# Optimization experiments

Measured on AMD Instinct MI355X. Metric: run time of the kernel, lower is better.

Reference implementation:

```python
import jax, jax.numpy as jnp
import numpy as np
from jax.scipy.special import i0

IM_SIZE = (256, 256)
GRID_SIZE = (512, 512)
NUMPOINTS = 6
OS = GRID_SIZE[0] / IM_SIZE[0]
# Beatty et al. optimal Kaiser-Bessel shape parameter
BETA = float(np.pi * np.sqrt((NUMPOINTS / OS) ** 2 * (OS - 0.5) ** 2 - 0.8))


def _apod_1d(N, G):
    # 1/FT(kb kernel) scaling coefficients (de-apodization), static numpy
    x = np.arange(N) - N / 2.0
    arg = np.pi * NUMPOINTS * x / G
    t = BETA ** 2 - arg ** 2  # > 0 for this config
    ph = np.sinh(np.sqrt(t)) / np.sqrt(t)
    return (1.0 / ph).astype(np.float32)


def _kb(u):
    # Kaiser-Bessel interpolation kernel, support |u| <= NUMPOINTS/2
    x = 2.0 * u / NUMPOINTS
    t = 1.0 - x * x
    inside = t > 0
    t = jnp.where(inside, t, 0.0)
    return jnp.where(inside, i0(BETA * jnp.sqrt(t)), 0.0)


def setup_inputs():
    key = jax.random.key(0)
    k1, k2, k3 = jax.random.split(key, 3)
    B, M = 8, 131072
    image = jax.random.normal(k1, (B,) + IM_SIZE, dtype=jnp.float32)
    ktraj = (jax.random.uniform(k2, (B, 2, M), dtype=jnp.float32) * 2.0 - 1.0) * jnp.pi
    dcf = jax.random.uniform(k3, (B, M), dtype=jnp.float32)
    return {"image": image, "ktraj": ktraj, "dcf": dcf}


def _nufft(image, ktraj, dcf):
    B = image.shape[0]
    N1, N2 = IM_SIZE
    G1, G2 = GRID_SIZE
    J = NUMPOINTS
    # 1) de-apodization (scaling coefficients), separable per-dim
    a1 = jnp.asarray(_apod_1d(N1, G1))
    a2 = jnp.asarray(_apod_1d(N2, G2))
    img = image.astype(jnp.complex64) * (a1[:, None] * a2[None, :])
    # 2) centered zero-pad to oversampled grid, FFT with DC at bin 0
    p1, p2 = (G1 - N1) // 2, (G2 - N2) // 2
    grid = jnp.zeros((B, G1, G2), dtype=jnp.complex64).at[:, p1:p1 + N1, p2:p2 + N2].set(img)
    kgrid = jnp.fft.fft2(jnp.fft.ifftshift(grid, axes=(1, 2)))
    # 3) KB interpolation (gather) at non-uniform points
    tm1 = ktraj[:, 0] * (G1 / (2.0 * jnp.pi))  # (B,M) in grid units
    tm2 = ktraj[:, 1] * (G2 / (2.0 * jnp.pi))
    offs = jnp.arange(J, dtype=jnp.float32) - (J // 2 - 1)  # [-2..3]
    g1 = jnp.floor(tm1)[..., None] + offs  # (B,M,J) neighbor coords
    g2 = jnp.floor(tm2)[..., None] + offs
    w1 = _kb(tm1[..., None] - g1)
    w2 = _kb(tm2[..., None] - g2)
    i1 = jnp.mod(g1.astype(jnp.int32), G1)
    i2 = jnp.mod(g2.astype(jnp.int32), G2)
    lin = (i1[..., :, None] * G2 + i2[..., None, :]).reshape(B, -1)  # (B, M*J*J)
    vals = jnp.take_along_axis(kgrid.reshape(B, -1), lin, axis=1).reshape(B, -1, J, J)
    w = (w1[..., :, None] * w2[..., None, :]).astype(jnp.complex64)
    kdata = jnp.sum(vals * w, axis=(-1, -2))  # (B,M) complex
    kdata = kdata * dcf
    return jnp.stack([kdata.real, kdata.imag], axis=0)  # (2,B,M) float32


def reference(image, ktraj, dcf):
    return _nufft(image, ktraj, dcf)
```

## Files before the change

kernel.cpp:

```cpp
#include <hip/hip_runtime.h>
#include <math.h>

#define GSZ 512
#define NSZ 256
#define NBATCH 8
#define MPTS 131072
#define PI_F 3.14159265358979f
#define BETA_F 13.8551004f
#define BETA2_F (BETA_F * BETA_F)
#define RSQ2 0.70710678f
#define PADIDX(i) ((i) + ((i) >> 3))


__device__ __forceinline__ float apod(int i) {
    float x = (float)(i - 128);
    float arg = PI_F * 6.0f * x * (1.0f / 512.0f);
    float t = BETA2_F - arg * arg;
    float st = sqrtf(t);
    return st / sinhf(st);
}

__device__ __forceinline__ float kbw(float u) {
    float t = 1.0f - u * u * (1.0f / 9.0f);
    float x = BETA_F * sqrtf(fmaxf(t, 0.0f));
    float xc = fmaxf(x, 0.35f);
    float r = __builtin_amdgcn_rcpf(xc);
    float poly = 1.0f + r * (0.125f + r * 0.0703125f);
    float w = __expf(xc) * __builtin_amdgcn_rsqf(6.2831853f * xc) * poly;
    return (t > 0.0f) ? w : 0.0f;
}

template<int CTRL>
__device__ __forceinline__ float qdpp(float v) {
    int r = __builtin_amdgcn_mov_dpp(__float_as_int(v), CTRL, 0xF, 0xF, true);
    return __int_as_float(r);
}

struct __align__(8) F4 { float x, y, z, w; };

__device__ __forceinline__ float2 cadd(float2 a, float2 b){ return make_float2(a.x+b.x, a.y+b.y); }
__device__ __forceinline__ float2 csub(float2 a, float2 b){ return make_float2(a.x-b.x, a.y-b.y); }
__device__ __forceinline__ float2 cmul(float2 a, float2 b){ return make_float2(a.x*b.x-a.y*b.y, a.x*b.y+a.y*b.x); }
__device__ __forceinline__ float2 mul_negi(float2 a){ return make_float2(a.y, -a.x); }
__device__ __forceinline__ float2 mul_posi(float2 a){ return make_float2(-a.y, a.x); }
__device__ __forceinline__ float2 mul_w81(float2 a){ return make_float2(RSQ2*(a.x+a.y), RSQ2*(a.y-a.x)); }
__device__ __forceinline__ float2 mul_w83(float2 a){ return make_float2(RSQ2*(a.y-a.x), -RSQ2*(a.x+a.y)); }

__device__ __forceinline__ void dft8_combine(float2 E0, float2 E1, float2 E2, float2 E3,
                                             float2 O0, float2 O1, float2 O2, float2 O3,
                                             float2* y) {
    float2 c1 = mul_w81(O1), c2 = mul_negi(O2), c3 = mul_w83(O3);
    y[0] = cadd(E0, O0); y[4] = csub(E0, O0);
    y[1] = cadd(E1, c1); y[5] = csub(E1, c1);
    y[2] = cadd(E2, c2); y[6] = csub(E2, c2);
    y[3] = cadd(E3, c3); y[7] = csub(E3, c3);
}

__device__ __forceinline__ void dft8(const float2* x, float2* y) {
    float2 a0=x[0], a1=x[2], a2=x[4], a3=x[6];
    float2 b0=x[1], b1=x[3], b2=x[5], b3=x[7];
    float2 ta0=cadd(a0,a2), ta1=csub(a0,a2), ta2=cadd(a1,a3), ta3=csub(a1,a3);
    float2 E0=cadd(ta0,ta2), E2=csub(ta0,ta2);
    float2 E1=cadd(ta1, mul_negi(ta3)), E3=cadd(ta1, mul_posi(ta3));
    float2 tb0=cadd(b0,b2), tb1=csub(b0,b2), tb2=cadd(b1,b3), tb3=csub(b1,b3);
    float2 O0=cadd(tb0,tb2), O2=csub(tb0,tb2);
    float2 O1=cadd(tb1, mul_negi(tb3)), O3=cadd(tb1, mul_posi(tb3));
    dft8_combine(E0,E1,E2,E3,O0,O1,O2,O3,y);
}

__device__ __forceinline__ void dft8_pruned(float2 x0, float2 x1, float2 x6, float2 x7, float2* y) {
    float2 E0 = cadd(x0, x6), E2 = csub(x0, x6);
    float2 E1 = cadd(x0, mul_posi(x6)), E3 = cadd(x0, mul_negi(x6));
    float2 O0 = cadd(x1, x7), O2 = csub(x1, x7);
    float2 O1 = cadd(x1, mul_posi(x7)), O3 = cadd(x1, mul_negi(x7));
    dft8_combine(E0,E1,E2,E3,O0,O1,O2,O3,y);
}

template<int S>
__device__ __forceinline__ void twiddle8(int t, float2* y) {
    if (S < 2) {
        int j = (S == 0) ? t : (t >> 3);
        const float scale = (S == 0) ? (-2.0f*PI_F/512.0f) : (-2.0f*PI_F/64.0f);
        float theta = scale * (float)j;
        float sn, cs;
        __sincosf(theta, &sn, &cs);
        float2 w = make_float2(cs, sn), wq = w;
        y[1] = cmul(y[1], wq);
        #pragma unroll
        for (int q = 2; q < 8; ++q) { wq = cmul(wq, w); y[q] = cmul(y[q], wq); }
    }
}

__global__ __launch_bounds__(256) void pass1_rowfft(const float* __restrict__ image,
                                                    float2* __restrict__ T) {
    __shared__ float2 sm[2][4][578];
    int tid = threadIdx.x;
    int r = tid >> 6, t = tid & 63;
    int blk = blockIdx.x;
    int b = blk & 7;
    int g = blk >> 3;
    int rp = (g << 2) + r;
    int y = (rp < 128) ? rp : (rp + 256);
    int iy = (y < 128) ? (y + 128) : (y - 384);
    float ay = apod(iy);
    const float* irow = image + ((size_t)(b * NSZ + iy)) * NSZ;

    float2 y8[8];
    {
        int ix0 = t + 128, ix1 = t + 192, ix6 = t, ix7 = t + 64;
        float2 x0 = make_float2(irow[ix0] * ay * apod(ix0), 0.f);
        float2 x1 = make_float2(irow[ix1] * ay * apod(ix1), 0.f);
        float2 x6 = make_float2(irow[ix6] * ay * apod(ix6), 0.f);
        float2 x7 = make_float2(irow[ix7] * ay * apod(ix7), 0.f);
        dft8_pruned(x0, x1, x6, x7, y8);
        twiddle8<0>(t, y8);
    }
    float2* A  = sm[0][r];
    float2* Bf = sm[1][r];
    #pragma unroll
    for (int q = 0; q < 8; ++q) A[PADIDX((t << 3) + q)] = y8[q];
    __syncthreads();
    {
        float2 x[8];
        #pragma unroll
        for (int p = 0; p < 8; ++p) x[p] = A[PADIDX(t + (p << 6))];
        dft8(x, y8);
        twiddle8<1>(t, y8);
        int j = t >> 3, k = t & 7, base = k + (j << 6);
        #pragma unroll
        for (int q = 0; q < 8; ++q) Bf[PADIDX(base + (q << 3))] = y8[q];
    }
    __syncthreads();
    {
        float2 x[8];
        #pragma unroll
        for (int p = 0; p < 8; ++p) x[p] = Bf[PADIDX(t + (p << 6))];
        dft8(x, y8);
        float2* Trow = T + (((size_t)(b << 8) + rp) << 9);
        #pragma unroll
        for (int q = 0; q < 8; ++q) Trow[t + (q << 6)] = y8[q];
    }
}

__global__ __launch_bounds__(256) void pass2_colfft(const float2* __restrict__ T,
                                                    float2* __restrict__ kgrid) {
    __shared__ float2 B[8][578];
    int tid = threadIdx.x;
    int blk = blockIdx.x;
    int b = blk & 7;
    int colbase = (blk >> 3) << 3;
    const float2* Tb = T + ((size_t)b << 17);
    float2* Kb = kgrid + ((size_t)b << 18);

    {
        int c = tid & 7, r0 = tid >> 3;
        #pragma unroll
        for (int k = 0; k < 8; ++k) {
            int rr = r0 + (k << 5);
            B[c][PADIDX(rr)] = Tb[((size_t)rr << 9) + colbase + c];
        }
    }
    __syncthreads();
    int t = tid & 63;
    int c0 = tid >> 6;
    float2 ya[8], yb[8];
    {
        float2* Ba = B[c0];
        float2* Bb = B[c0 + 4];
        float2 a0 = Ba[PADIDX(t)],   a1 = Ba[PADIDX(t + 64)];
        float2 a6 = Ba[PADIDX(t + 128)], a7 = Ba[PADIDX(t + 192)];
        float2 b0 = Bb[PADIDX(t)],   b1 = Bb[PADIDX(t + 64)];
        float2 b6 = Bb[PADIDX(t + 128)], b7 = Bb[PADIDX(t + 192)];
        dft8_pruned(a0, a1, a6, a7, ya); twiddle8<0>(t, ya);
        dft8_pruned(b0, b1, b6, b7, yb); twiddle8<0>(t, yb);
    }
    __syncthreads();
    #pragma unroll
    for (int q = 0; q < 8; ++q) {
        B[c0][PADIDX((t << 3) + q)]     = ya[q];
        B[c0 + 4][PADIDX((t << 3) + q)] = yb[q];
    }
    __syncthreads();
    {
        float2 xa[8], xb[8];
        #pragma unroll
        for (int p = 0; p < 8; ++p) { xa[p] = B[c0][PADIDX(t + (p << 6))]; xb[p] = B[c0 + 4][PADIDX(t + (p << 6))]; }
        dft8(xa, ya); twiddle8<1>(t, ya);
        dft8(xb, yb); twiddle8<1>(t, yb);
    }
    __syncthreads();
    {
        int j = t >> 3, k = t & 7, base = k + (j << 6);
        #pragma unroll
        for (int q = 0; q < 8; ++q) {
            B[c0][PADIDX(base + (q << 3))]     = ya[q];
            B[c0 + 4][PADIDX(base + (q << 3))] = yb[q];
        }
    }
    __syncthreads();
    {
        float2 xa[8], xb[8];
        #pragma unroll
        for (int p = 0; p < 8; ++p) { xa[p] = B[c0][PADIDX(t + (p << 6))]; xb[p] = B[c0 + 4][PADIDX(t + (p << 6))]; }
        dft8(xa, ya);
        dft8(xb, yb);
    }
    __syncthreads();
    #pragma unroll
    for (int q = 0; q < 8; ++q) {
        B[c0][PADIDX(t + (q << 6))]     = ya[q];
        B[c0 + 4][PADIDX(t + (q << 6))] = yb[q];
    }
    __syncthreads();
    {
        int c = tid & 7, r0 = tid >> 3;
        #pragma unroll
        for (int k = 0; k < 16; ++k) {
            int rr = r0 + (k << 5);
            Kb[((size_t)rr << 9) + colbase + c] = B[c][PADIDX(rr)];
        }
    }
}

__global__ __launch_bounds__(256) void interp_kb(const float* __restrict__ ktraj,
                                                 const float* __restrict__ dcf,
                                                 const float2* __restrict__ kgrid,
                                                 float* __restrict__ out) {
    int tid = threadIdx.x;
    int blk = blockIdx.x;
    int b = blk & 7;
    int gb = blk >> 3;
    int j = tid & 3;
    int q = tid >> 2;

    const float SCALE = (float)GSZ / (2.0f * PI_F);
    const float2* Kb = kgrid + ((size_t)b << 18);
    const float* kt1 = ktraj + ((size_t)(b * 2)) * MPTS;
    const float* kt2 = kt1 + MPTS;
    const float* dcfb = dcf + ((size_t)b << 17);
    float* out_re = out + ((size_t)b << 17);
    float* out_im = out_re + (size_t)NBATCH * MPTS;

    int m0 = (gb << 9) + q;
    #pragma unroll 2
    for (int it = 0; it < 8; ++it) {
        int m = m0 + (it << 6);
        float tm1 = kt1[m] * SCALE;
        float tm2 = kt2[m] * SCALE;
        float f1 = floorf(tm1), f2 = floorf(tm2);
        int if1 = (int)f1, if2 = (int)f2;
        int e0 = (if2 - 2) & ~1;

        float u2 = tm2 - (float)(e0 + 2 * j);
        float w2a = kbw(u2);
        float w2b = kbw(u2 - 1.0f);
        int cpair = (e0 + 2 * j) & 511;

        float fr1 = tm1 - f1;
        float w1A = kbw(fr1 - (float)(j - 2));
        float w1B = kbw(fr1 - (float)(j + 2));

        float c0re = 0.f, c0im = 0.f, c1re = 0.f, c1im = 0.f;
        #define KB_ROW(a, W, CTRL)                                            \
        {                                                                     \
            float w1a = qdpp<CTRL>(W);                                        \
            int rowb = (if1 + (a) - 2) & 511;                                 \
            F4 v = *reinterpret_cast<const F4*>(Kb + ((size_t)rowb << 9) + cpair); \
            c0re = fmaf(w1a, v.x, c0re); c0im = fmaf(w1a, v.y, c0im);         \
            c1re = fmaf(w1a, v.z, c1re); c1im = fmaf(w1a, v.w, c1im);         \
        }
        KB_ROW(0, w1A, 0x00)
        KB_ROW(1, w1A, 0x55)
        KB_ROW(2, w1A, 0xAA)
        KB_ROW(3, w1A, 0xFF)
        KB_ROW(4, w1B, 0x00)
        KB_ROW(5, w1B, 0x55)
        #undef KB_ROW

        float p_re = fmaf(w2a, c0re, w2b * c1re);
        float p_im = fmaf(w2a, c0im, w2b * c1im);
        p_re += qdpp<0xB1>(p_re);  p_re += qdpp<0x4E>(p_re);
        p_im += qdpp<0xB1>(p_im);  p_im += qdpp<0x4E>(p_im);

        float dd = dcfb[m];
        if (j == 0) out_re[m] = p_re * dd;
        if (j == 1) out_im[m] = p_im * dd;
    }
}


extern "C" void kernel_launch(void* const* d_in, const int* in_sizes, int n_in,
                              void* d_out, int out_size, void* d_ws, size_t ws_size,
                              hipStream_t stream) {
    const float* image = (const float*)d_in[0];
    const float* ktraj = (const float*)d_in[1];
    const float* dcf   = (const float*)d_in[2];
    float* out = (float*)d_out;

    float2* T     = (float2*)d_ws;
    float2* kgrid = T + (size_t)NBATCH * 256 * GSZ;

    pass1_rowfft<<<NBATCH * 64, 256, 0, stream>>>(image, T);
    pass2_colfft<<<NBATCH * 64, 256, 0, stream>>>(T, kgrid);
    interp_kb<<<NBATCH * 256, 256, 0, stream>>>(ktraj, dcf, kgrid, out);
}
```

Measured before the change: 128.5 us.

## Fuse row FFT, column FFT and interpolation into one persistent kernel

Merges the three launches into a single kernel of 512 blocks. Per-batch software barriers built on global atomic counters replace the kernel boundaries between the row FFT, column FFT and KB gather stages. Each block now interpolates four times as many points as before. The aim is to remove launch gaps and tail effects between stages. The risks are deadlock if the 64 blocks of a batch are not all co-resident, the cost of spinning on the barrier, and lower parallelism in the interpolation stage (512 blocks instead of 2048).

```diff
diff --git a/kernel.cpp b/kernel.cpp
--- a/kernel.cpp
+++ b/kernel.cpp
@@ -10,6 +10,27 @@
 #define BETA2_F (BETA_F * BETA_F)
 #define RSQ2 0.70710678f
 #define PADIDX(i) ((i) + ((i) >> 3))
+
+struct __align__(128) BatchBar { unsigned cnt; unsigned gen; unsigned pad[30]; };
+__device__ BatchBar g_bar[NBATCH];
+
+__device__ __forceinline__ void batch_sync(int b) {
+    __syncthreads();
+    if (threadIdx.x == 0) {
+        __threadfence();
+        unsigned g = __hip_atomic_load(&g_bar[b].gen, __ATOMIC_RELAXED, __HIP_MEMORY_SCOPE_AGENT);
+        unsigned a = __hip_atomic_fetch_add(&g_bar[b].cnt, 1u, __ATOMIC_ACQ_REL, __HIP_MEMORY_SCOPE_AGENT);
+        if (a == 63u) {
+            __hip_atomic_store(&g_bar[b].cnt, 0u, __ATOMIC_RELAXED, __HIP_MEMORY_SCOPE_AGENT);
+            __hip_atomic_fetch_add(&g_bar[b].gen, 1u, __ATOMIC_RELEASE, __HIP_MEMORY_SCOPE_AGENT);
+        } else {
+            while (__hip_atomic_load(&g_bar[b].gen, __ATOMIC_ACQUIRE, __HIP_MEMORY_SCOPE_AGENT) == g)
+                __builtin_amdgcn_s_sleep(2);
+        }
+        __threadfence();
+    }
+    __syncthreads();
+}
 
 
 __device__ __forceinline__ float apod(int i) {
@@ -91,200 +112,200 @@
     }
 }
 
-__global__ __launch_bounds__(256) void pass1_rowfft(const float* __restrict__ image,
-                                                    float2* __restrict__ T) {
-    __shared__ float2 sm[2][4][578];
+__global__ __launch_bounds__(256, 2) void nufft_fused(const float* __restrict__ image,
+                                                      const float* __restrict__ ktraj,
+                                                      const float* __restrict__ dcf,
+                                                      float2* __restrict__ T,
+                                                      float2* __restrict__ kgrid,
+                                                      float* __restrict__ out) {
+    __shared__ float2 smem[8 * 578];
     int tid = threadIdx.x;
-    int r = tid >> 6, t = tid & 63;
     int blk = blockIdx.x;
     int b = blk & 7;
     int g = blk >> 3;
-    int rp = (g << 2) + r;
-    int y = (rp < 128) ? rp : (rp + 256);
-    int iy = (y < 128) ? (y + 128) : (y - 384);
-    float ay = apod(iy);
-    const float* irow = image + ((size_t)(b * NSZ + iy)) * NSZ;
-
-    float2 y8[8];
+
     {
-        int ix0 = t + 128, ix1 = t + 192, ix6 = t, ix7 = t + 64;
-        float2 x0 = make_float2(irow[ix0] * ay * apod(ix0), 0.f);
-        float2 x1 = make_float2(irow[ix1] * ay * apod(ix1), 0.f);
-        float2 x6 = make_float2(irow[ix6] * ay * apod(ix6), 0.f);
-        float2 x7 = make_float2(irow[ix7] * ay * apod(ix7), 0.f);
-        dft8_pruned(x0, x1, x6, x7, y8);
-        twiddle8<0>(t, y8);
-    }
-    float2* A  = sm[0][r];
-    float2* Bf = sm[1][r];
-    #pragma unroll
-    for (int q = 0; q < 8; ++q) A[PADIDX((t << 3) + q)] = y8[q];
-    __syncthreads();
+        int r = tid >> 6, t = tid & 63;
+        int rp = (g << 2) + r;
+        int y = (rp < 128) ? rp : (rp + 256);
+        int iy = (y < 128) ? (y + 128) : (y - 384);
+        float ay = apod(iy);
+        const float* irow = image + ((size_t)(b * NSZ + iy)) * NSZ;
+
+        float2 y8[8];
+        {
+            int ix0 = t + 128, ix1 = t + 192, ix6 = t, ix7 = t + 64;
+            float2 x0 = make_float2(irow[ix0] * ay * apod(ix0), 0.f);
+            float2 x1 = make_float2(irow[ix1] * ay * apod(ix1), 0.f);
+            float2 x6 = make_float2(irow[ix6] * ay * apod(ix6), 0.f);
+            float2 x7 = make_float2(irow[ix7] * ay * apod(ix7), 0.f);
+            dft8_pruned(x0, x1, x6, x7, y8);
+            twiddle8<0>(t, y8);
+        }
+        float2* A  = smem + r * 578;
+        float2* Bf = smem + (r + 4) * 578;
+        #pragma unroll
+        for (int q = 0; q < 8; ++q) A[PADIDX((t << 3) + q)] = y8[q];
+        __syncthreads();
+        {
+            float2 x[8];
+            #pragma unroll
+            for (int p = 0; p < 8; ++p) x[p] = A[PADIDX(t + (p << 6))];
+            dft8(x, y8);
+            twiddle8<1>(t, y8);
+            int j = t >> 3, k = t & 7, base = k + (j << 6);
+            #pragma unroll
+            for (int q = 0; q < 8; ++q) Bf[PADIDX(base + (q << 3))] = y8[q];
+        }
+        __syncthreads();
+        {
+            float2 x[8];
+            #pragma unroll
+            for (int p = 0; p < 8; ++p) x[p] = Bf[PADIDX(t + (p << 6))];
+            dft8(x, y8);
+            float2* Trow = T + (((size_t)(b << 8) + rp) << 9);
+            #pragma unroll
+            for (int q = 0; q < 8; ++q) Trow[t + (q << 6)] = y8[q];
+        }
+    }
+
+    batch_sync(b);
+
     {
-        float2 x[8];
-        #pragma unroll
-        for (int p = 0; p < 8; ++p) x[p] = A[PADIDX(t + (p << 6))];
-        dft8(x, y8);
-        twiddle8<1>(t, y8);
-        int j = t >> 3, k = t & 7, base = k + (j << 6);
-        #pragma unroll
-        for (int q = 0; q < 8; ++q) Bf[PADIDX(base + (q << 3))] = y8[q];
-    }
-    __syncthreads();
-    {
-        float2 x[8];
-        #pragma unroll
-        for (int p = 0; p < 8; ++p) x[p] = Bf[PADIDX(t + (p << 6))];
-        dft8(x, y8);
-        float2* Trow = T + (((size_t)(b << 8) + rp) << 9);
-        #pragma unroll
-        for (int q = 0; q < 8; ++q) Trow[t + (q << 6)] = y8[q];
-    }
-}
-
-__global__ __launch_bounds__(256) void pass2_colfft(const float2* __restrict__ T,
-                                                    float2* __restrict__ kgrid) {
-    __shared__ float2 B[8][578];
-    int tid = threadIdx.x;
-    int blk = blockIdx.x;
-    int b = blk & 7;
-    int colbase = (blk >> 3) << 3;
-    const float2* Tb = T + ((size_t)b << 17);
-    float2* Kb = kgrid + ((size_t)b << 18);
-
-    {
-        int c = tid & 7, r0 = tid >> 3;
-        #pragma unroll
-        for (int k = 0; k < 8; ++k) {
-            int rr = r0 + (k << 5);
-            B[c][PADIDX(rr)] = Tb[((size_t)rr << 9) + colbase + c];
-        }
-    }
-    __syncthreads();
-    int t = tid & 63;
-    int c0 = tid >> 6;
-    float2 ya[8], yb[8];
-    {
-        float2* Ba = B[c0];
-        float2* Bb = B[c0 + 4];
-        float2 a0 = Ba[PADIDX(t)],   a1 = Ba[PADIDX(t + 64)];
-        float2 a6 = Ba[PADIDX(t + 128)], a7 = Ba[PADIDX(t + 192)];
-        float2 b0 = Bb[PADIDX(t)],   b1 = Bb[PADIDX(t + 64)];
-        float2 b6 = Bb[PADIDX(t + 128)], b7 = Bb[PADIDX(t + 192)];
-        dft8_pruned(a0, a1, a6, a7, ya); twiddle8<0>(t, ya);
-        dft8_pruned(b0, b1, b6, b7, yb); twiddle8<0>(t, yb);
-    }
-    __syncthreads();
-    #pragma unroll
-    for (int q = 0; q < 8; ++q) {
-        B[c0][PADIDX((t << 3) + q)]     = ya[q];
-        B[c0 + 4][PADIDX((t << 3) + q)] = yb[q];
-    }
-    __syncthreads();
-    {
-        float2 xa[8], xb[8];
-        #pragma unroll
-        for (int p = 0; p < 8; ++p) { xa[p] = B[c0][PADIDX(t + (p << 6))]; xb[p] = B[c0 + 4][PADIDX(t + (p << 6))]; }
-        dft8(xa, ya); twiddle8<1>(t, ya);
-        dft8(xb, yb); twiddle8<1>(t, yb);
-    }
-    __syncthreads();
-    {
-        int j = t >> 3, k = t & 7, base = k + (j << 6);
+        int colbase = g << 3;
+        const float2* Tb = T + ((size_t)b << 17);
+        float2* Kb = kgrid + ((size_t)b << 18);
+        float2* B0 = smem;
+
+        {
+            int c = tid & 7, r0 = tid >> 3;
+            #pragma unroll
+            for (int k = 0; k < 8; ++k) {
+                int rr = r0 + (k << 5);
+                B0[c * 578 + PADIDX(rr)] = Tb[((size_t)rr << 9) + colbase + c];
+            }
+        }
+        __syncthreads();
+        int t = tid & 63;
+        int c0 = tid >> 6;
+        float2* Ba = B0 + c0 * 578;
+        float2* Bb = B0 + (c0 + 4) * 578;
+        float2 ya[8], yb[8];
+        {
+            float2 a0 = Ba[PADIDX(t)],     a1 = Ba[PADIDX(t + 64)];
+            float2 a6 = Ba[PADIDX(t + 128)], a7 = Ba[PADIDX(t + 192)];
+            float2 b0 = Bb[PADIDX(t)],     b1 = Bb[PADIDX(t + 64)];
+            float2 b6 = Bb[PADIDX(t + 128)], b7 = Bb[PADIDX(t + 192)];
+            dft8_pruned(a0, a1, a6, a7, ya); twiddle8<0>(t, ya);
+            dft8_pruned(b0, b1, b6, b7, yb); twiddle8<0>(t, yb);
+        }
+        __syncthreads();
         #pragma unroll
         for (int q = 0; q < 8; ++q) {
-            B[c0][PADIDX(base + (q << 3))]     = ya[q];
-            B[c0 + 4][PADIDX(base + (q << 3))] = yb[q];
-        }
-    }
-    __syncthreads();
+            Ba[PADIDX((t << 3) + q)] = ya[q];
+            Bb[PADIDX((t << 3) + q)] = yb[q];
+        }
+        __syncthreads();
+        {
+            float2 xa[8], xb[8];
+            #pragma unroll
+            for (int p = 0; p < 8; ++p) { xa[p] = Ba[PADIDX(t + (p << 6))]; xb[p] = Bb[PADIDX(t + (p << 6))]; }
+            dft8(xa, ya); twiddle8<1>(t, ya);
+            dft8(xb, yb); twiddle8<1>(t, yb);
+        }
+        __syncthreads();
+        {
+            int j = t >> 3, k = t & 7, base = k + (j << 6);
+            #pragma unroll
+            for (int q = 0; q < 8; ++q) {
+                Ba[PADIDX(base + (q << 3))] = ya[q];
+                Bb[PADIDX(base + (q << 3))] = yb[q];
+            }
+        }
+        __syncthreads();
+        {
+            float2 xa[8], xb[8];
+            #pragma unroll
+            for (int p = 0; p < 8; ++p) { xa[p] = Ba[PADIDX(t + (p << 6))]; xb[p] = Bb[PADIDX(t + (p << 6))]; }
+            dft8(xa, ya);
+            dft8(xb, yb);
+        }
+        __syncthreads();
+        #pragma unroll
+        for (int q = 0; q < 8; ++q) {
+            Ba[PADIDX(t + (q << 6))] = ya[q];
+            Bb[PADIDX(t + (q << 6))] = yb[q];
+        }
+        __syncthreads();
+        {
+            int c = tid & 7, r0 = tid >> 3;
+            #pragma unroll
+            for (int k = 0; k < 16; ++k) {
+                int rr = r0 + (k << 5);
+                Kb[((size_t)rr << 9) + colbase + c] = B0[c * 578 + PADIDX(rr)];
+            }
+        }
+    }
+
+    batch_sync(b);
+
     {
-        float2 xa[8], xb[8];
-        #pragma unroll
-        for (int p = 0; p < 8; ++p) { xa[p] = B[c0][PADIDX(t + (p << 6))]; xb[p] = B[c0 + 4][PADIDX(t + (p << 6))]; }
-        dft8(xa, ya);
-        dft8(xb, yb);
-    }
-    __syncthreads();
-    #pragma unroll
-    for (int q = 0; q < 8; ++q) {
-        B[c0][PADIDX(t + (q << 6))]     = ya[q];
-        B[c0 + 4][PADIDX(t + (q << 6))] = yb[q];
-    }
-    __syncthreads();
-    {
-        int c = tid & 7, r0 = tid >> 3;
-        #pragma unroll
-        for (int k = 0; k < 16; ++k) {
-            int rr = r0 + (k << 5);
-            Kb[((size_t)rr << 9) + colbase + c] = B[c][PADIDX(rr)];
-        }
-    }
-}
-
-__global__ __launch_bounds__(256) void interp_kb(const float* __restrict__ ktraj,
-                                                 const float* __restrict__ dcf,
-                                                 const float2* __restrict__ kgrid,
-                                                 float* __restrict__ out) {
-    int tid = threadIdx.x;
-    int blk = blockIdx.x;
-    int b = blk & 7;
-    int gb = blk >> 3;
-    int j = tid & 3;
-    int q = tid >> 2;
-
-    const float SCALE = (float)GSZ / (2.0f * PI_F);
-    const float2* Kb = kgrid + ((size_t)b << 18);
-    const float* kt1 = ktraj + ((size_t)(b * 2)) * MPTS;
-    const float* kt2 = kt1 + MPTS;
-    const float* dcfb = dcf + ((size_t)b << 17);
-    float* out_re = out + ((size_t)b << 17);
-    float* out_im = out_re + (size_t)NBATCH * MPTS;
-
-    int m0 = (gb << 9) + q;
-    #pragma unroll 2
-    for (int it = 0; it < 8; ++it) {
-        int m = m0 + (it << 6);
-        float tm1 = kt1[m] * SCALE;
-        float tm2 = kt2[m] * SCALE;
-        float f1 = floorf(tm1), f2 = floorf(tm2);
-        int if1 = (int)f1, if2 = (int)f2;
-        int e0 = (if2 - 2) & ~1;
-
-        float u2 = tm2 - (float)(e0 + 2 * j);
-        float w2a = kbw(u2);
-        float w2b = kbw(u2 - 1.0f);
-        int cpair = (e0 + 2 * j) & 511;
-
-        float fr1 = tm1 - f1;
-        float w1A = kbw(fr1 - (float)(j - 2));
-        float w1B = kbw(fr1 - (float)(j + 2));
-
-        float c0re = 0.f, c0im = 0.f, c1re = 0.f, c1im = 0.f;
-        #define KB_ROW(a, W, CTRL)                                            \
-        {                                                                     \
-            float w1a = qdpp<CTRL>(W);                                        \
-            int rowb = (if1 + (a) - 2) & 511;                                 \
-            F4 v = *reinterpret_cast<const F4*>(Kb + ((size_t)rowb << 9) + cpair); \
-            c0re = fmaf(w1a, v.x, c0re); c0im = fmaf(w1a, v.y, c0im);         \
-            c1re = fmaf(w1a, v.z, c1re); c1im = fmaf(w1a, v.w, c1im);         \
-        }
-        KB_ROW(0, w1A, 0x00)
-        KB_ROW(1, w1A, 0x55)
-        KB_ROW(2, w1A, 0xAA)
-        KB_ROW(3, w1A, 0xFF)
-        KB_ROW(4, w1B, 0x00)
-        KB_ROW(5, w1B, 0x55)
-        #undef KB_ROW
-
-        float p_re = fmaf(w2a, c0re, w2b * c1re);
-        float p_im = fmaf(w2a, c0im, w2b * c1im);
-        p_re += qdpp<0xB1>(p_re);  p_re += qdpp<0x4E>(p_re);
-        p_im += qdpp<0xB1>(p_im);  p_im += qdpp<0x4E>(p_im);
-
-        float dd = dcfb[m];
-        if (j == 0) out_re[m] = p_re * dd;
-        if (j == 1) out_im[m] = p_im * dd;
+        int j = tid & 3;
+        int q = tid >> 2;
+
+        const float SCALE = (float)GSZ / (2.0f * PI_F);
+        const float2* Kb = kgrid + ((size_t)b << 18);
+        const float* kt1 = ktraj + ((size_t)(b * 2)) * MPTS;
+        const float* kt2 = kt1 + MPTS;
+        const float* dcfb = dcf + ((size_t)b << 17);
+        float* out_re = out + ((size_t)b << 17);
+        float* out_im = out_re + (size_t)NBATCH * MPTS;
+
+        int m0 = (g << 11) + q;
+        #pragma unroll 2
+        for (int it = 0; it < 32; ++it) {
+            int m = m0 + (it << 6);
+            float tm1 = kt1[m] * SCALE;
+            float tm2 = kt2[m] * SCALE;
+            float f1 = floorf(tm1), f2 = floorf(tm2);
+            int if1 = (int)f1, if2 = (int)f2;
+            int e0 = (if2 - 2) & ~1;
+
+            float u2 = tm2 - (float)(e0 + 2 * j);
+            float w2a = kbw(u2);
+            float w2b = kbw(u2 - 1.0f);
+            int cpair = (e0 + 2 * j) & 511;
+
+            float fr1 = tm1 - f1;
+            float w1A = kbw(fr1 - (float)(j - 2));
+            float w1B = kbw(fr1 - (float)(j + 2));
+
+            float c0re = 0.f, c0im = 0.f, c1re = 0.f, c1im = 0.f;
+            #define KB_ROW(a, W, CTRL)                                            \
+            {                                                                     \
+                float w1a = qdpp<CTRL>(W);                                        \
+                int rowb = (if1 + (a) - 2) & 511;                                 \
+                F4 v = *reinterpret_cast<const F4*>(Kb + ((size_t)rowb << 9) + cpair); \
+                c0re = fmaf(w1a, v.x, c0re); c0im = fmaf(w1a, v.y, c0im);         \
+                c1re = fmaf(w1a, v.z, c1re); c1im = fmaf(w1a, v.w, c1im);         \
+            }
+            KB_ROW(0, w1A, 0x00)
+            KB_ROW(1, w1A, 0x55)
+            KB_ROW(2, w1A, 0xAA)
+            KB_ROW(3, w1A, 0xFF)
+            KB_ROW(4, w1B, 0x00)
+            KB_ROW(5, w1B, 0x55)
+            #undef KB_ROW
+
+            float p_re = fmaf(w2a, c0re, w2b * c1re);
+            float p_im = fmaf(w2a, c0im, w2b * c1im);
+            p_re += qdpp<0xB1>(p_re);  p_re += qdpp<0x4E>(p_re);
+            p_im += qdpp<0xB1>(p_im);  p_im += qdpp<0x4E>(p_im);
+
+            float dd = dcfb[m];
+            if (j == 0) out_re[m] = p_re * dd;
+            if (j == 1) out_im[m] = p_im * dd;
+        }
     }
 }
 
@@ -300,7 +321,5 @@
     float2* T     = (float2*)d_ws;
     float2* kgrid = T + (size_t)NBATCH * 256 * GSZ;
 
-    pass1_rowfft<<<NBATCH * 64, 256, 0, stream>>>(image, T);
-    pass2_colfft<<<NBATCH * 64, 256, 0, stream>>>(T, kgrid);
-    interp_kb<<<NBATCH * 256, 256, 0, stream>>>(ktraj, dcf, kgrid, out);
-}
+    nufft_fused<<<NBATCH * 64, 256, 0, stream>>>(image, ktraj, dcf, T, kgrid, out);
+}
```

After: 245.8 us. 91.2% more time.

## Pack two real images per complex FFT and separate spectra via Hermitian symmetry

Applied to the files above, without the earlier changes.

Because each input image is real, two batch images are loaded as the real and imaginary parts of one complex signal. This halves the row and column FFT work and the intermediate buffer. The column pass computes mirrored column pairs and splits the two spectra through conjugate symmetry before writing both grids, with special handling for the DC and Nyquist columns. The Kaiser-Bessel weight's asymptotic polynomial is also rewritten in rsqrt form, which drops the separate reciprocal. The cost is more complicated index mapping and fewer, smaller blocks in the FFT passes.

```diff
diff --git a/kernel.cpp b/kernel.cpp
--- a/kernel.cpp
+++ b/kernel.cpp
@@ -24,9 +24,10 @@
     float t = 1.0f - u * u * (1.0f / 9.0f);
     float x = BETA_F * sqrtf(fmaxf(t, 0.0f));
     float xc = fmaxf(x, 0.35f);
-    float r = __builtin_amdgcn_rcpf(xc);
-    float poly = 1.0f + r * (0.125f + r * 0.0703125f);
-    float w = __expf(xc) * __builtin_amdgcn_rsqf(6.2831853f * xc) * poly;
+    float R = __builtin_amdgcn_rsqf(xc);
+    float R2 = R * R;
+    float q = R * (0.39894228f + R2 * (0.04986779f + R2 * 0.02804702f));
+    float w = __expf(xc) * q;
     return (t > 0.0f) ? w : 0.0f;
 }
 
@@ -91,27 +92,30 @@
     }
 }
 
-__global__ __launch_bounds__(256) void pass1_rowfft(const float* __restrict__ image,
+__global__ __launch_bounds__(128) void pass1_rowfft(const float* __restrict__ image,
                                                     float2* __restrict__ T) {
-    __shared__ float2 sm[2][4][578];
+    __shared__ float2 sm[2][2][578];
     int tid = threadIdx.x;
     int r = tid >> 6, t = tid & 63;
     int blk = blockIdx.x;
-    int b = blk & 7;
-    int g = blk >> 3;
-    int rp = (g << 2) + r;
+    int p = blk & 3;
+    int g = blk >> 2;
+    int rp = (g << 1) + r;
     int y = (rp < 128) ? rp : (rp + 256);
     int iy = (y < 128) ? (y + 128) : (y - 384);
     float ay = apod(iy);
-    const float* irow = image + ((size_t)(b * NSZ + iy)) * NSZ;
+    const float* irow0 = image + ((size_t)((2 * p)     * NSZ + iy)) * NSZ;
+    const float* irow1 = image + ((size_t)((2 * p + 1) * NSZ + iy)) * NSZ;
 
     float2 y8[8];
     {
         int ix0 = t + 128, ix1 = t + 192, ix6 = t, ix7 = t + 64;
-        float2 x0 = make_float2(irow[ix0] * ay * apod(ix0), 0.f);
-        float2 x1 = make_float2(irow[ix1] * ay * apod(ix1), 0.f);
-        float2 x6 = make_float2(irow[ix6] * ay * apod(ix6), 0.f);
-        float2 x7 = make_float2(irow[ix7] * ay * apod(ix7), 0.f);
+        float w0 = ay * apod(ix0), w1 = ay * apod(ix1);
+        float w6 = ay * apod(ix6), w7 = ay * apod(ix7);
+        float2 x0 = make_float2(irow0[ix0] * w0, irow1[ix0] * w0);
+        float2 x1 = make_float2(irow0[ix1] * w1, irow1[ix1] * w1);
+        float2 x6 = make_float2(irow0[ix6] * w6, irow1[ix6] * w6);
+        float2 x7 = make_float2(irow0[ix7] * w7, irow1[ix7] * w7);
         dft8_pruned(x0, x1, x6, x7, y8);
         twiddle8<0>(t, y8);
     }
@@ -123,7 +127,7 @@
     {
         float2 x[8];
         #pragma unroll
-        for (int p = 0; p < 8; ++p) x[p] = A[PADIDX(t + (p << 6))];
+        for (int pp = 0; pp < 8; ++pp) x[pp] = A[PADIDX(t + (pp << 6))];
         dft8(x, y8);
         twiddle8<1>(t, y8);
         int j = t >> 3, k = t & 7, base = k + (j << 6);
@@ -134,9 +138,9 @@
     {
         float2 x[8];
         #pragma unroll
-        for (int p = 0; p < 8; ++p) x[p] = Bf[PADIDX(t + (p << 6))];
+        for (int pp = 0; pp < 8; ++pp) x[pp] = Bf[PADIDX(t + (pp << 6))];
         dft8(x, y8);
-        float2* Trow = T + (((size_t)(b << 8) + rp) << 9);
+        float2* Trow = T + (((size_t)(p << 8) + rp) << 9);
         #pragma unroll
         for (int q = 0; q < 8; ++q) Trow[t + (q << 6)] = y8[q];
     }
@@ -147,29 +151,34 @@
     __shared__ float2 B[8][578];
     int tid = threadIdx.x;
     int blk = blockIdx.x;
-    int b = blk & 7;
-    int colbase = (blk >> 3) << 3;
-    const float2* Tb = T + ((size_t)b << 17);
-    float2* Kb = kgrid + ((size_t)b << 18);
+    int p = blk & 3;
+    int g = blk >> 2;
+    const float2* Tb = T + ((size_t)p << 17);
+    float2* Kb0 = kgrid + ((size_t)(2 * p) << 18);
+    float2* Kb1 = Kb0 + ((size_t)1 << 18);
+
+    #define COLG(c) ((g > 0) ? (((c) < 4) ? ((g << 2) + (c)) : (505 - (g << 2) + (c))) \
+                             : (((c) < 4) ? (c) : (((c) == 7) ? 256 : (505 + (c)))))
 
     {
         int c = tid & 7, r0 = tid >> 3;
+        int colg = COLG(c);
         #pragma unroll
         for (int k = 0; k < 8; ++k) {
             int rr = r0 + (k << 5);
-            B[c][PADIDX(rr)] = Tb[((size_t)rr << 9) + colbase + c];
+            B[c][PADIDX(rr)] = Tb[((size_t)rr << 9) + colg];
         }
     }
     __syncthreads();
     int t = tid & 63;
     int c0 = tid >> 6;
+    float2* Ba = B[c0];
+    float2* Bb = B[c0 + 4];
     float2 ya[8], yb[8];
     {
-        float2* Ba = B[c0];
-        float2* Bb = B[c0 + 4];
-        float2 a0 = Ba[PADIDX(t)],   a1 = Ba[PADIDX(t + 64)];
+        float2 a0 = Ba[PADIDX(t)],       a1 = Ba[PADIDX(t + 64)];
         float2 a6 = Ba[PADIDX(t + 128)], a7 = Ba[PADIDX(t + 192)];
-        float2 b0 = Bb[PADIDX(t)],   b1 = Bb[PADIDX(t + 64)];
+        float2 b0 = Bb[PADIDX(t)],       b1 = Bb[PADIDX(t + 64)];
         float2 b6 = Bb[PADIDX(t + 128)], b7 = Bb[PADIDX(t + 192)];
         dft8_pruned(a0, a1, a6, a7, ya); twiddle8<0>(t, ya);
         dft8_pruned(b0, b1, b6, b7, yb); twiddle8<0>(t, yb);
@@ -177,14 +186,14 @@
     __syncthreads();
     #pragma unroll
     for (int q = 0; q < 8; ++q) {
-        B[c0][PADIDX((t << 3) + q)]     = ya[q];
-        B[c0 + 4][PADIDX((t << 3) + q)] = yb[q];
+        Ba[PADIDX((t << 3) + q)] = ya[q];
+        Bb[PADIDX((t << 3) + q)] = yb[q];
     }
     __syncthreads();
     {
         float2 xa[8], xb[8];
         #pragma unroll
-        for (int p = 0; p < 8; ++p) { xa[p] = B[c0][PADIDX(t + (p << 6))]; xb[p] = B[c0 + 4][PADIDX(t + (p << 6))]; }
+        for (int pp = 0; pp < 8; ++pp) { xa[pp] = Ba[PADIDX(t + (pp << 6))]; xb[pp] = Bb[PADIDX(t + (pp << 6))]; }
         dft8(xa, ya); twiddle8<1>(t, ya);
         dft8(xb, yb); twiddle8<1>(t, yb);
     }
@@ -193,33 +202,44 @@
         int j = t >> 3, k = t & 7, base = k + (j << 6);
         #pragma unroll
         for (int q = 0; q < 8; ++q) {
-            B[c0][PADIDX(base + (q << 3))]     = ya[q];
-            B[c0 + 4][PADIDX(base + (q << 3))] = yb[q];
+            Ba[PADIDX(base + (q << 3))] = ya[q];
+            Bb[PADIDX(base + (q << 3))] = yb[q];
         }
     }
     __syncthreads();
     {
         float2 xa[8], xb[8];
         #pragma unroll
-        for (int p = 0; p < 8; ++p) { xa[p] = B[c0][PADIDX(t + (p << 6))]; xb[p] = B[c0 + 4][PADIDX(t + (p << 6))]; }
+        for (int pp = 0; pp < 8; ++pp) { xa[pp] = Ba[PADIDX(t + (pp << 6))]; xb[pp] = Bb[PADIDX(t + (pp << 6))]; }
         dft8(xa, ya);
         dft8(xb, yb);
     }
     __syncthreads();
     #pragma unroll
     for (int q = 0; q < 8; ++q) {
-        B[c0][PADIDX(t + (q << 6))]     = ya[q];
-        B[c0 + 4][PADIDX(t + (q << 6))] = yb[q];
+        Ba[PADIDX(t + (q << 6))] = ya[q];
+        Bb[PADIDX(t + (q << 6))] = yb[q];
     }
     __syncthreads();
     {
         int c = tid & 7, r0 = tid >> 3;
+        int colg = COLG(c);
+        int mc = 7 - c;
+        if (g == 0) { if (c == 0) mc = 0; else if (c == 7) mc = 7; }
         #pragma unroll
         for (int k = 0; k < 16; ++k) {
             int rr = r0 + (k << 5);
-            Kb[((size_t)rr << 9) + colbase + c] = B[c][PADIDX(rr)];
+            int mr = (512 - rr) & 511;
+            float2 Z = B[c][PADIDX(rr)];
+            float2 M = B[mc][PADIDX(mr)];
+            float2 K0 = make_float2(0.5f * (Z.x + M.x), 0.5f * (Z.y - M.y));
+            float2 K1 = make_float2(0.5f * (Z.y + M.y), 0.5f * (M.x - Z.x));
+            size_t off = ((size_t)rr << 9) + colg;
+            Kb0[off] = K0;
+            Kb1[off] = K1;
         }
     }
+    #undef COLG
 }
 
 __global__ __launch_bounds__(256) void interp_kb(const float* __restrict__ ktraj,
@@ -298,9 +318,9 @@
     float* out = (float*)d_out;
 
     float2* T     = (float2*)d_ws;
-    float2* kgrid = T + (size_t)NBATCH * 256 * GSZ;
-
-    pass1_rowfft<<<NBATCH * 64, 256, 0, stream>>>(image, T);
-    pass2_colfft<<<NBATCH * 64, 256, 0, stream>>>(T, kgrid);
+    float2* kgrid = T + (size_t)4 * 256 * GSZ;
+
+    pass1_rowfft<<<512, 128, 0, stream>>>(image, T);
+    pass2_colfft<<<256, 256, 0, stream>>>(T, kgrid);
     interp_kb<<<NBATCH * 256, 256, 0, stream>>>(ktraj, dcf, kgrid, out);
 }
```

Measured after the change: 130.7 us. About the same (+1.7%).
